# Kernel optimization log

Measured on AMD Instinct MI355X. Metric: run time of the kernel, lower is better.

## Reference

```python
import jax, jax.numpy as jnp
import numpy as np

B, N, C = 2, 2048, 256
H_DIM, W_DIM = 64, 176


def _lin_init(k, fan_in, shape):
    return jax.random.normal(k, shape, dtype=jnp.float32) * (1.0 / np.sqrt(fan_in))


def setup_inputs() -> dict:
    key = jax.random.key(0)
    ks = jax.random.split(key, 12)
    # gaussian_data: (B, N, 14); positions [:3], sigma_x at 5, sigma_y at 6, weight at 12
    z = jax.random.uniform(ks[0], (B, N), minval=1.0, maxval=40.0)
    x = jax.random.uniform(ks[1], (B, N), minval=-0.6, maxval=0.6) * z
    y = jax.random.uniform(ks[2], (B, N), minval=-0.4, maxval=0.4) * z
    g = jax.random.normal(ks[3], (B, N, 14), dtype=jnp.float32)
    g = g.at[..., 0].set(x).at[..., 1].set(y).at[..., 2].set(z)
    g = g.at[..., 5].set(jax.random.uniform(ks[4], (B, N), minval=5.0, maxval=50.0))
    g = g.at[..., 6].set(jax.random.uniform(ks[5], (B, N), minval=5.0, maxval=50.0))
    g = g.at[..., 12].set(jax.random.uniform(ks[6], (B, N), minval=0.5, maxval=1.5))
    # pinhole intrinsic: fx=fy=1000, cx=880, cy=320
    intrinsic = jnp.array([[1000.0, 0.0, 880.0], [0.0, 1000.0, 320.0], [0.0, 0.0, 1.0]], dtype=jnp.float32)
    pk = jax.random.split(ks[7], 5)
    return {
        "gaussian_data": g,
        "intrinsic": intrinsic,
        "enc_w1": _lin_init(pk[0], 14, (14, 64)), "enc_b1": jnp.zeros((64,), jnp.float32),
        "enc_w2": _lin_init(pk[1], 64, (64, 128)), "enc_b2": jnp.zeros((128,), jnp.float32),
        "enc_w3": _lin_init(pk[2], 128, (128, C)), "enc_b3": jnp.zeros((C,), jnp.float32),
        "ft_w1": _lin_init(pk[3], C, (C, C)), "ft_b1": jnp.zeros((C,), jnp.float32),
        "ft_w2": _lin_init(pk[4], C, (C, C)), "ft_b2": jnp.zeros((C,), jnp.float32),
        "H": H_DIM, "W": W_DIM,
    }


def reference(gaussian_data, intrinsic, enc_w1, enc_b1, enc_w2, enc_b2, enc_w3, enc_b3,
              ft_w1, ft_b1, ft_w2, ft_b2, H, W):
    # Encoder MLP (dropout = identity in eval): (B,N,14) -> (B,N,C)
    h = jax.nn.relu(gaussian_data @ enc_w1 + enc_b1)
    h = jax.nn.relu(h @ enc_w2 + enc_b2)
    feats = h @ enc_w3 + enc_b3
    # feature_transform inside GaussianRadarProjection
    feats_t = jax.nn.relu(feats @ ft_w1 + ft_b1) @ ft_w2 + ft_b2  # (B,N,C)

    pos = gaussian_data[..., :3]                      # (B,N,3)
    valid = pos[..., 2] > 0.1                         # (B,N)
    proj = jnp.einsum('ij,bnj->bni', intrinsic, pos)  # (B,N,3)
    pts2d = proj[..., :2] / (proj[..., 2:3] + 1e-6)   # (B,N,2)
    scale_x = W / intrinsic[0, 2] / 2
    scale_y = H / intrinsic[1, 2] / 2
    px = pts2d[..., 0] * scale_x                      # (B,N)
    py = pts2d[..., 1] * scale_y
    inb = (px >= 0) & (px < W) & (py >= 0) & (py < H)
    mask = valid & inb                                # (B,N)

    sx = jnp.maximum(gaussian_data[..., 5] * scale_x, 1.0)  # (B,N)
    sy = jnp.maximum(gaussian_data[..., 6] * scale_y, 1.0)
    w = gaussian_data[..., 12]                               # (B,N)

    xg = jnp.arange(W, dtype=jnp.float32)
    yg = jnp.arange(H, dtype=jnp.float32)
    dx2 = ((xg[None, None, :] - px[..., None]) / sx[..., None]) ** 2  # (B,N,W)
    dy2 = ((yg[None, None, :] - py[..., None]) / sy[..., None]) ** 2  # (B,N,H)
    dist = dy2[..., :, None] + dx2[..., None, :]                      # (B,N,H,W)
    gw = jnp.exp(-0.5 * dist) * w[..., None, None]
    gw = gw * (dist < 9.0).astype(gw.dtype) * mask[..., None, None].astype(gw.dtype)

    density = jnp.sum(gw, axis=1)[:, None]                             # (B,1,H,W)
    feature_map = jnp.einsum('bnc,bnhw->bchw', feats_t, gw)            # (B,C,H,W)
    avg_sigma = (sx + sy) / 2                                          # (B,N)
    uncertainty = jnp.sum(gw * avg_sigma[..., None, None], axis=1)[:, None]

    density = jnp.clip(density, 1e-6)
    return feature_map / density, uncertainty / density, density
```

## Files before the change

### kernel.cpp

```cpp
#include <hip/hip_runtime.h>
#include <cstdint>
#include <cstddef>

#define B_ 2
#define N_ 2048
#define C_ 256
#define H_ 64
#define W_ 176
#define TW 16
#define NTX 11
#define NYB 32
#define NTILES2 (B_*NYB*NTX)
#define NSUB 8
#define SUBCAP 256
#define SA 260
#define FS 40
#define CSTRIDE 16

typedef unsigned short ushort_t;
typedef short bf16x8 __attribute__((ext_vector_type(8)));
typedef float f32x4  __attribute__((ext_vector_type(4)));

__device__ __forceinline__ short f2bf(float f)
{
    unsigned u = __float_as_uint(f);
    return (short)((u + 0x7FFFu + ((u >> 16) & 1u)) >> 16);
}

__global__ __launch_bounds__(256)
void prep_kernel(const float* __restrict__ w3f, const float* __restrict__ fw1f,
                 const float* __restrict__ fw2f,
                 short* __restrict__ wt3, short* __restrict__ wt4,
                 short* __restrict__ wt5, int* __restrict__ counts)
{
    const int gid = blockIdx.x * 256 + threadIdx.x;
    for (int c = gid; c < NTILES2 * NSUB * CSTRIDE; c += 65536) counts[c] = 0;
    for (int e = gid; e < 163840; e += 65536) {
        if (e < 32768) {
            const int k = e >> 8, n = e & 255;
            wt3[n * 128 + k] = f2bf(w3f[e]);
        } else if (e < 98304) {
            const int e2 = e - 32768;
            const int k = e2 >> 8, n = e2 & 255;
            wt4[n * 256 + k] = f2bf(fw1f[e2]);
        } else {
            const int e2 = e - 98304;
            const int k = e2 >> 8, n = e2 & 255;
            wt5[n * 256 + k] = f2bf(fw2f[e2]);
        }
    }
}

template<int K>
__device__ __forceinline__ void mfma_acc(const short* __restrict__ wt,
                                         const float* actIn, f32x4 (&acc)[2],
                                         int wv_, int quad, int ln15)
{
    bf16x8 wreg[K / 16];
#pragma unroll
    for (int ks = 0; ks < K / 32; ++ks) {
        const int kb = ks * 32 + quad * 8;
#pragma unroll
        for (int tt = 0; tt < 2; ++tt) {
            const int n0 = (wv_ * 2 + tt) * 16;
            wreg[ks * 2 + tt] = *(const bf16x8*)&wt[(size_t)(n0 + ln15) * K + kb];
        }
    }
#pragma unroll
    for (int ks = 0; ks < K / 32; ++ks) {
        const int kb = ks * 32 + quad * 8;
        const float4 a0 = *(const float4*)&actIn[ln15 * SA + kb];
        const float4 a1 = *(const float4*)&actIn[ln15 * SA + kb + 4];
        bf16x8 af = { f2bf(a0.x), f2bf(a0.y), f2bf(a0.z), f2bf(a0.w),
                      f2bf(a1.x), f2bf(a1.y), f2bf(a1.z), f2bf(a1.w) };
#pragma unroll
        for (int tt = 0; tt < 2; ++tt)
            acc[tt] = __builtin_amdgcn_mfma_f32_16x16x32_bf16(af, wreg[ks * 2 + tt],
                                                              acc[tt], 0, 0, 0);
    }
}

__global__ __launch_bounds__(512, 4)
void pb_mlp_kernel(const float* __restrict__ g, const float* __restrict__ intr,
                   const float* __restrict__ w1, const float* __restrict__ b1,
                   const float* __restrict__ w2, const float* __restrict__ b2,
                   const short* __restrict__ wt3, const float* __restrict__ b3,
                   const short* __restrict__ wt4, const float* __restrict__ fb1,
                   const short* __restrict__ wt5, const float* __restrict__ fb2,
                   ushort_t* __restrict__ ftb,
                   float* __restrict__ pp, int* __restrict__ counts,
                   ushort_t* __restrict__ lists)
{
    __shared__ __align__(16) float A_[16 * SA];
    __shared__ __align__(16) float Bb[16 * SA];
    const int tid = threadIdx.x;

    if (blockIdx.x < 256) {
        const int row0 = blockIdx.x * 16;
        const int lane = tid & 63;
        const int wv_  = tid >> 6;
        const int quad = lane >> 4;
        const int ln15 = lane & 15;

        if (tid < 224) {
            const int k = tid / 16, m = tid % 16;
            A_[m * SA + k] = g[(size_t)(row0 + m) * 14 + k];
        }
        __syncthreads();

        {
            const int col = tid & 63;
            const int m0  = (tid >> 6) * 2;
            float acc[2];
            const float bv = b1[col];
            acc[0] = bv; acc[1] = bv;
#pragma unroll
            for (int k = 0; k < 14; ++k) {
                const float wv = w1[k * 64 + col];
                acc[0] = fmaf(A_[(m0 + 0) * SA + k], wv, acc[0]);
                acc[1] = fmaf(A_[(m0 + 1) * SA + k], wv, acc[1]);
            }
            Bb[(m0 + 0) * SA + col] = fmaxf(acc[0], 0.f);
            Bb[(m0 + 1) * SA + col] = fmaxf(acc[1], 0.f);
        }
        __syncthreads();

        {
            const int col = tid & 127;
            const int m0  = (tid >> 7) * 4;
            float acc[4];
            const float bv = b2[col];
#pragma unroll
            for (int r = 0; r < 4; ++r) acc[r] = bv;
#pragma unroll 4
            for (int kq = 0; kq < 16; ++kq) {
                float wv[4];
#pragma unroll
                for (int jj = 0; jj < 4; ++jj) wv[jj] = w2[(4 * kq + jj) * 128 + col];
#pragma unroll
                for (int r = 0; r < 4; ++r) {
                    const float4 a4 = *(const float4*)&Bb[(m0 + r) * SA + 4 * kq];
                    acc[r] = fmaf(a4.x, wv[0], acc[r]);
                    acc[r] = fmaf(a4.y, wv[1], acc[r]);
                    acc[r] = fmaf(a4.z, wv[2], acc[r]);
                    acc[r] = fmaf(a4.w, wv[3], acc[r]);
                }
            }
#pragma unroll
            for (int r = 0; r < 4; ++r)
                A_[(m0 + r) * SA + col] = fmaxf(acc[r], 0.f);
        }
        __syncthreads();

        {
            f32x4 acc[2] = {{0,0,0,0},{0,0,0,0}};
            mfma_acc<128>(wt3, A_, acc, wv_, quad, ln15);
            __syncthreads();
#pragma unroll
            for (int tt = 0; tt < 2; ++tt) {
                const int n = (wv_ * 2 + tt) * 16 + ln15;
                const float bv = b3[n];
#pragma unroll
                for (int r = 0; r < 4; ++r)
                    Bb[(quad * 4 + r) * SA + n] = acc[tt][r] + bv;
            }
        }
        __syncthreads();

        {
            f32x4 acc[2] = {{0,0,0,0},{0,0,0,0}};
            mfma_acc<256>(wt4, Bb, acc, wv_, quad, ln15);
            __syncthreads();
#pragma unroll
            for (int tt = 0; tt < 2; ++tt) {
                const int n = (wv_ * 2 + tt) * 16 + ln15;
                const float bv = fb1[n];
#pragma unroll
                for (int r = 0; r < 4; ++r)
                    A_[(quad * 4 + r) * SA + n] = fmaxf(acc[tt][r] + bv, 0.f);
            }
        }
        __syncthreads();

        {
            f32x4 acc[2] = {{0,0,0,0},{0,0,0,0}};
            mfma_acc<256>(wt5, A_, acc, wv_, quad, ln15);
#pragma unroll
            for (int tt = 0; tt < 2; ++tt) {
                const int n = (wv_ * 2 + tt) * 16 + ln15;
                const float bv = fb2[n];
#pragma unroll
                for (int r = 0; r < 4; ++r)
                    ftb[(size_t)(row0 + quad * 4 + r) * 256 + n] =
                        (ushort_t)f2bf(acc[tt][r] + bv);
            }
        }
        return;
    }

    const int sub = (blockIdx.x - 256) & (NSUB - 1);
    const int i = (blockIdx.x - 256) * 16 + (tid >> 5);
    const int j = tid & 31;
    const float* gi = g + (size_t)i * 14;
    const float x = gi[0], y = gi[1], z = gi[2];
    const float s5 = gi[5], s6 = gi[6], wv = gi[12];
    const float k00 = intr[0], k01 = intr[1], k02 = intr[2];
    const float k10 = intr[3], k11 = intr[4], k12 = intr[5];
    const float k20 = intr[6], k21 = intr[7], k22 = intr[8];
    const float projx = k00 * x + k01 * y + k02 * z;
    const float projy = k10 * x + k11 * y + k12 * z;
    const float projz = k20 * x + k21 * y + k22 * z;
    const float inv = 1.f / (projz + 1e-6f);
    const float scale_x = (float)W_ / k02 * 0.5f;
    const float scale_y = (float)H_ / k12 * 0.5f;
    const float px = projx * inv * scale_x;
    const float py = projy * inv * scale_y;
    const bool valid = z > 0.1f;
    const bool inb = (px >= 0.f) && (px < (float)W_) && (py >= 0.f) && (py < (float)H_);
    const bool mask = valid && inb;
    const float sx = fmaxf(s5 * scale_x, 1.f);
    const float sy = fmaxf(s6 * scale_y, 1.f);
    if (j == 0) {
        float4* o = (float4*)(pp + (size_t)i * 8);
        o[0] = make_float4(px, py, 1.f / sx, 1.f / sy);
        o[1] = make_float4(wv, 0.5f * (sx + sy), 0.f, 0.f);
    }
    if (!mask) return;
    const float rx = 3.f * sx, ry = 3.f * sy;
    const int ymin = max(0, (int)floorf(py - ry));
    const int ymax = min(H_ - 1, (int)ceilf(py + ry));
    const int bmin = ymin >> 1, bmax = ymax >> 1;
    const int band = bmin + j;
    if (band > bmax) return;
    const int tmin = max(0, (int)floorf((px - rx - (float)(TW - 1)) * (1.f / TW)));
    const int tmax = min(NTX - 1, (int)ceilf((px + rx) * (1.f / TW)));
    const int b = i / N_, n = i - b * N_;
    for (int t = tmin; t <= tmax; ++t) {
        const int tile = (b * NYB + band) * NTX + t;
        const int slot = atomicAdd(&counts[(tile * NSUB + sub) * CSTRIDE], 1);
        if (slot < SUBCAP)
            lists[((size_t)tile * NSUB + sub) * SUBCAP + slot] = (ushort_t)n;
    }
}

__global__ __launch_bounds__(512)
void splat_kernel(const float* __restrict__ pp, const ushort_t* __restrict__ lists,
                  const int* __restrict__ counts, const ushort_t* __restrict__ ftb,
                  float* __restrict__ out)
{
    __shared__ __align__(16) ushort_t feats_t[2][256 * FS];
    __shared__ __align__(16) ushort_t gw_t[2][32 * FS];
    __shared__ __align__(16) ushort_t list_s[NSUB * SUBCAP];

    const int tid = threadIdx.x;
    const int qb = blockIdx.x;
    const int b  = qb & 1;
    const int t_ = qb >> 1;
    const int yr = t_ / NTX, xr = t_ % NTX;
    const int yh = (yr + 1) >> 1;
    const int yb = (yr & 1) ? (16 - yh) : (16 + yh);
    const int xh = (xr + 1) >> 1;
    const int txi = (xr & 1) ? (5 - xh) : (5 + xh);
    const int tb  = (b * NYB + yb) * NTX + txi;
    const int y0 = yb * 2, x0 = txi * TW;

    int cs[NSUB];
#pragma unroll
    for (int s = 0; s < NSUB; ++s)
        cs[s] = min(counts[(tb * NSUB + s) * CSTRIDE], SUBCAP);
    int off[NSUB];
    int tot = 0;
#pragma unroll
    for (int s = 0; s < NSUB; ++s) { off[s] = tot; tot += cs[s]; }
#pragma unroll
    for (int s = 0; s < NSUB; ++s) {
        const ushort_t* src = lists + ((size_t)tb * NSUB + s) * SUBCAP;
        if (tid < cs[s]) list_s[off[s] + tid] = src[tid];
    }
    __syncthreads();
    const int cnt = tot;

    const ushort_t* mylist = list_s;
    const int gs   = tid >> 5;
    const int px32 = tid & 31;
    const float fy = (float)(y0 + (px32 >> 4));
    const float fx = (float)(x0 + (px32 & 15));
    const int chg = tid >> 4;
    const int qp  = tid & 15;
    const int bN = b * N_;
    const int lane = tid & 63;
    const int wv_  = tid >> 6;
    const int quad = lane >> 4;
    const int ln15 = lane & 15;

    f32x4 acc[2][2];
#pragma unroll
    for (int mt = 0; mt < 2; ++mt)
#pragma unroll
        for (int nt = 0; nt < 2; ++nt) acc[mt][nt] = (f32x4){0.f, 0.f, 0.f, 0.f};
    float densp = 0.f, uncp = 0.f;

    uint4 ra0, rb0;
    const int nchunks = (cnt + 31) >> 5;

    if (cnt > 0) {
        const float4* pv = (const float4*)pp;
        {
            const int n0 = mylist[min(2 * qp, cnt - 1)];
            const int n1 = mylist[min(2 * qp + 1, cnt - 1)];
            ra0 = *(const uint4*)(ftb + ((size_t)(bN + n0) << 8) + chg * 8);
            rb0 = *(const uint4*)(ftb + ((size_t)(bN + n1) << 8) + chg * 8);
        }
        for (int c = 0; c < nchunks; ++c) {
            const int buf = c & 1;
#pragma unroll
            for (int jj = 0; jj < 2; ++jj) {
                const int q = 16 * jj + gs;
                const int qi = c * 32 + q;
                const int n = mylist[min(qi, cnt - 1)];
                const float4 e0 = pv[(size_t)(bN + n) * 2 + 0];
                const float4 e1 = pv[(size_t)(bN + n) * 2 + 1];
                const float dyn = (fy - e0.y) * e0.w;
                const float dxn = (fx - e0.x) * e0.z;
                const float dist = dyn * dyn + dxn * dxn;
                float gv = 0.f;
                if (dist < 9.f) gv = __expf(-0.5f * dist) * e1.x;
                if (qi >= cnt) gv = 0.f;
                gw_t[buf][px32 * FS + q] = (ushort_t)f2bf(gv);
                densp += gv;
                uncp  += gv * e1.y;
            }
            {
                uint* dst = (uint*)&feats_t[buf][0];
#pragma unroll
                for (int jj = 0; jj < 4; ++jj) {
                    const uint u0 = (&ra0.x)[jj], v0 = (&rb0.x)[jj];
                    const int ch = chg * 8 + 2 * jj;
                    dst[ch * (FS / 2) + qp]       = (u0 & 0xffffu) | (v0 << 16);
                    dst[(ch + 1) * (FS / 2) + qp] = (u0 >> 16) | (v0 & 0xffff0000u);
                }
            }
            __syncthreads();
            if (c + 1 < nchunks) {
                const int q0 = (c + 1) * 32 + 2 * qp;
                const int n0 = mylist[min(q0, cnt - 1)];
                const int n1 = mylist[min(q0 + 1, cnt - 1)];
                ra0 = *(const uint4*)(ftb + ((size_t)(bN + n0) << 8) + chg * 8);
                rb0 = *(const uint4*)(ftb + ((size_t)(bN + n1) << 8) + chg * 8);
            }
            bf16x8 af[2];
#pragma unroll
            for (int mt = 0; mt < 2; ++mt)
                af[mt] = *(const bf16x8*)&gw_t[buf][(mt * 16 + ln15) * FS + quad * 8];
#pragma unroll
            for (int nt = 0; nt < 2; ++nt) {
                const int ch0 = wv_ * 32 + nt * 16;
                const bf16x8 bf = *(const bf16x8*)&feats_t[buf][(ch0 + ln15) * FS + quad * 8];
                acc[0][nt] = __builtin_amdgcn_mfma_f32_16x16x32_bf16(af[0], bf, acc[0][nt], 0, 0, 0);
                acc[1][nt] = __builtin_amdgcn_mfma_f32_16x16x32_bf16(af[1], bf, acc[1][nt], 0, 0, 0);
            }
        }
    }

    __syncthreads();
    float* red_d = (float*)&feats_t[0][0];
    float* red_u = red_d + 16 * 36;
    red_d[gs * 36 + px32] = densp;
    red_u[gs * 36 + px32] = uncp;
    __syncthreads();
    for (int s = 8; s > 0; s >>= 1) {
        if (gs < s) {
            red_d[gs * 36 + px32] += red_d[(gs + s) * 36 + px32];
            red_u[gs * 36 + px32] += red_u[(gs + s) * 36 + px32];
        }
        __syncthreads();
    }

    if (tid < 32) {
        const int yy = y0 + (tid >> 4), xx = x0 + (tid & 15);
        const size_t pix = ((size_t)b * H_ + yy) * W_ + xx;
        float* unc_o = out + (size_t)B_ * C_ * H_ * W_;
        float* den_o = unc_o + (size_t)B_ * H_ * W_;
        const float d = fmaxf(red_d[tid], 1e-6f);
        unc_o[pix] = red_u[tid] / d;
        den_o[pix] = d;
    }

#pragma unroll
    for (int mt = 0; mt < 2; ++mt) {
        const int pxb = mt * 16 + quad * 4;
        float rinv[4];
#pragma unroll
        for (int r = 0; r < 4; ++r)
            rinv[r] = 1.f / fmaxf(red_d[pxb + r], 1e-6f);
        const int yy = y0 + mt;
#pragma unroll
        for (int nt = 0; nt < 2; ++nt) {
            const int ch = wv_ * 32 + nt * 16 + ln15;
            float4 v;
            v.x = acc[mt][nt][0] * rinv[0];
            v.y = acc[mt][nt][1] * rinv[1];
            v.z = acc[mt][nt][2] * rinv[2];
            v.w = acc[mt][nt][3] * rinv[3];
            *(float4*)(out + (((size_t)b * C_ + ch) * H_ + yy) * W_
                       + x0 + quad * 4) = v;
        }
    }
}

extern "C" void kernel_launch(void* const* d_in, const int* in_sizes, int n_in,
                              void* d_out, int out_size, void* d_ws, size_t ws_size,
                              hipStream_t stream)
{
    const float* g    = (const float*)d_in[0];
    const float* intr = (const float*)d_in[1];
    const float* w1   = (const float*)d_in[2];
    const float* b1   = (const float*)d_in[3];
    const float* w2   = (const float*)d_in[4];
    const float* b2   = (const float*)d_in[5];
    const float* w3   = (const float*)d_in[6];
    const float* b3   = (const float*)d_in[7];
    const float* fw1  = (const float*)d_in[8];
    const float* fb1  = (const float*)d_in[9];
    const float* fw2  = (const float*)d_in[10];
    const float* fb2  = (const float*)d_in[11];

    char* base = (char*)d_ws;
    const int rows = B_ * N_;
    ushort_t* ftb = (ushort_t*)base;
    float* pp     = (float*)(base + (size_t)rows * C_ * 2);
    int*   counts = (int*)(pp + (size_t)8 * rows);
    ushort_t* lists = (ushort_t*)(counts + NTILES2 * NSUB * CSTRIDE);
    short* wt3    = (short*)(lists + (size_t)NTILES2 * NSUB * SUBCAP);
    short* wt4    = wt3 + 128 * 256;
    short* wt5    = wt4 + 256 * 256;

    prep_kernel<<<dim3(256), dim3(256), 0, stream>>>(w3, fw1, fw2, wt3, wt4, wt5, counts);
    pb_mlp_kernel<<<dim3(512), dim3(512), 0, stream>>>(
        g, intr, w1, b1, w2, b2, wt3, b3, wt4, fb1, wt5, fb2, ftb, pp, counts, lists);
    splat_kernel<<<dim3(NTILES2), dim3(512), 0, stream>>>(pp, lists, counts, ftb, (float*)d_out);
}
```

Measured before the change: 128.8 us.

## Store MLP activations as bf16 in LDS and deepen splat prefetch pipeline

The MLP kernel now keeps its intermediate activations in shared memory as bf16 with a padded stride. This removes the per-load float-to-bf16 conversions and halves the LDS footprint, which also lets two __syncthreads calls be dropped. The splat kernel gains a 4-wave occupancy hint and prefetches feature rows two chunks ahead with register double-buffering. It also prefetches the next chunk's gaussian parameters into registers while the current chunk is being processed. The extra in-flight registers may cost occupancy, and the drop from two barriers to one between MLP stages depends on the separate buffer alternation being safe.

```diff
diff --git a/kernel.cpp b/kernel.cpp
--- a/kernel.cpp
+++ b/kernel.cpp
@@ -13,9 +13,9 @@
 #define NTILES2 (B_*NYB*NTX)
 #define NSUB 8
 #define SUBCAP 256
-#define SA 260
 #define FS 40
 #define CSTRIDE 16
+#define SAB 264
 
 typedef unsigned short ushort_t;
 typedef short bf16x8 __attribute__((ext_vector_type(8)));
@@ -52,9 +52,9 @@
 }
 
 template<int K>
-__device__ __forceinline__ void mfma_acc(const short* __restrict__ wt,
-                                         const float* actIn, f32x4 (&acc)[2],
-                                         int wv_, int quad, int ln15)
+__device__ __forceinline__ void mfma_accB(const short* __restrict__ wt,
+                                          const ushort_t* actB, f32x4 (&acc)[2],
+                                          int wv_, int quad, int ln15)
 {
     bf16x8 wreg[K / 16];
 #pragma unroll
@@ -69,10 +69,7 @@
 #pragma unroll
     for (int ks = 0; ks < K / 32; ++ks) {
         const int kb = ks * 32 + quad * 8;
-        const float4 a0 = *(const float4*)&actIn[ln15 * SA + kb];
-        const float4 a1 = *(const float4*)&actIn[ln15 * SA + kb + 4];
-        bf16x8 af = { f2bf(a0.x), f2bf(a0.y), f2bf(a0.z), f2bf(a0.w),
-                      f2bf(a1.x), f2bf(a1.y), f2bf(a1.z), f2bf(a1.w) };
+        const bf16x8 af = *(const bf16x8*)&actB[ln15 * SAB + kb];
 #pragma unroll
         for (int tt = 0; tt < 2; ++tt)
             acc[tt] = __builtin_amdgcn_mfma_f32_16x16x32_bf16(af, wreg[ks * 2 + tt],
@@ -91,8 +88,10 @@
                    float* __restrict__ pp, int* __restrict__ counts,
                    ushort_t* __restrict__ lists)
 {
-    __shared__ __align__(16) float A_[16 * SA];
-    __shared__ __align__(16) float Bb[16 * SA];
+    __shared__ __align__(16) float   s32a[16 * 16];
+    __shared__ __align__(16) float   s32b[16 * 68];
+    __shared__ __align__(16) ushort_t bA[16 * SAB];
+    __shared__ __align__(16) ushort_t bB[16 * SAB];
     const int tid = threadIdx.x;
 
     if (blockIdx.x < 256) {
@@ -104,7 +103,7 @@
 
         if (tid < 224) {
             const int k = tid / 16, m = tid % 16;
-            A_[m * SA + k] = g[(size_t)(row0 + m) * 14 + k];
+            s32a[m * 16 + k] = g[(size_t)(row0 + m) * 14 + k];
         }
         __syncthreads();
 
@@ -117,11 +116,11 @@
 #pragma unroll
             for (int k = 0; k < 14; ++k) {
                 const float wv = w1[k * 64 + col];
-                acc[0] = fmaf(A_[(m0 + 0) * SA + k], wv, acc[0]);
-                acc[1] = fmaf(A_[(m0 + 1) * SA + k], wv, acc[1]);
-            }
-            Bb[(m0 + 0) * SA + col] = fmaxf(acc[0], 0.f);
-            Bb[(m0 + 1) * SA + col] = fmaxf(acc[1], 0.f);
+                acc[0] = fmaf(s32a[(m0 + 0) * 16 + k], wv, acc[0]);
+                acc[1] = fmaf(s32a[(m0 + 1) * 16 + k], wv, acc[1]);
+            }
+            s32b[(m0 + 0) * 68 + col] = fmaxf(acc[0], 0.f);
+            s32b[(m0 + 1) * 68 + col] = fmaxf(acc[1], 0.f);
         }
         __syncthreads();
 
@@ -139,7 +138,7 @@
                 for (int jj = 0; jj < 4; ++jj) wv[jj] = w2[(4 * kq + jj) * 128 + col];
 #pragma unroll
                 for (int r = 0; r < 4; ++r) {
-                    const float4 a4 = *(const float4*)&Bb[(m0 + r) * SA + 4 * kq];
+                    const float4 a4 = *(const float4*)&s32b[(m0 + r) * 68 + 4 * kq];
                     acc[r] = fmaf(a4.x, wv[0], acc[r]);
                     acc[r] = fmaf(a4.y, wv[1], acc[r]);
                     acc[r] = fmaf(a4.z, wv[2], acc[r]);
@@ -148,43 +147,42 @@
             }
 #pragma unroll
             for (int r = 0; r < 4; ++r)
-                A_[(m0 + r) * SA + col] = fmaxf(acc[r], 0.f);
+                bA[(m0 + r) * SAB + col] = (ushort_t)f2bf(fmaxf(acc[r], 0.f));
         }
         __syncthreads();
 
         {
             f32x4 acc[2] = {{0,0,0,0},{0,0,0,0}};
-            mfma_acc<128>(wt3, A_, acc, wv_, quad, ln15);
-            __syncthreads();
+            mfma_accB<128>(wt3, bA, acc, wv_, quad, ln15);
 #pragma unroll
             for (int tt = 0; tt < 2; ++tt) {
                 const int n = (wv_ * 2 + tt) * 16 + ln15;
                 const float bv = b3[n];
 #pragma unroll
                 for (int r = 0; r < 4; ++r)
-                    Bb[(quad * 4 + r) * SA + n] = acc[tt][r] + bv;
+                    bB[(quad * 4 + r) * SAB + n] = (ushort_t)f2bf(acc[tt][r] + bv);
             }
         }
         __syncthreads();
 
         {
             f32x4 acc[2] = {{0,0,0,0},{0,0,0,0}};
-            mfma_acc<256>(wt4, Bb, acc, wv_, quad, ln15);
-            __syncthreads();
+            mfma_accB<256>(wt4, bB, acc, wv_, quad, ln15);
 #pragma unroll
             for (int tt = 0; tt < 2; ++tt) {
                 const int n = (wv_ * 2 + tt) * 16 + ln15;
                 const float bv = fb1[n];
 #pragma unroll
                 for (int r = 0; r < 4; ++r)
-                    A_[(quad * 4 + r) * SA + n] = fmaxf(acc[tt][r] + bv, 0.f);
+                    bA[(quad * 4 + r) * SAB + n] =
+                        (ushort_t)f2bf(fmaxf(acc[tt][r] + bv, 0.f));
             }
         }
         __syncthreads();
 
         {
             f32x4 acc[2] = {{0,0,0,0},{0,0,0,0}};
-            mfma_acc<256>(wt5, A_, acc, wv_, quad, ln15);
+            mfma_accB<256>(wt5, bA, acc, wv_, quad, ln15);
 #pragma unroll
             for (int tt = 0; tt < 2; ++tt) {
                 const int n = (wv_ * 2 + tt) * 16 + ln15;
@@ -243,7 +241,7 @@
     }
 }
 
-__global__ __launch_bounds__(512)
+__global__ __launch_bounds__(512, 4)
 void splat_kernel(const float* __restrict__ pp, const ushort_t* __restrict__ lists,
                   const int* __restrict__ counts, const ushort_t* __restrict__ ftb,
                   float* __restrict__ out)
@@ -280,7 +278,6 @@
     __syncthreads();
     const int cnt = tot;
 
-    const ushort_t* mylist = list_s;
     const int gs   = tid >> 5;
     const int px32 = tid & 31;
     const float fy = (float)(y0 + (px32 >> 4));
@@ -300,26 +297,40 @@
         for (int nt = 0; nt < 2; ++nt) acc[mt][nt] = (f32x4){0.f, 0.f, 0.f, 0.f};
     float densp = 0.f, uncp = 0.f;
 
-    uint4 ra0, rb0;
+    uint4 fa[2], fb[2];
+    float4 pe0[2], pe1[2];
     const int nchunks = (cnt + 31) >> 5;
 
     if (cnt > 0) {
         const float4* pv = (const float4*)pp;
         {
-            const int n0 = mylist[min(2 * qp, cnt - 1)];
-            const int n1 = mylist[min(2 * qp + 1, cnt - 1)];
-            ra0 = *(const uint4*)(ftb + ((size_t)(bN + n0) << 8) + chg * 8);
-            rb0 = *(const uint4*)(ftb + ((size_t)(bN + n1) << 8) + chg * 8);
-        }
+            const int n0 = list_s[min(2 * qp, cnt - 1)];
+            const int n1 = list_s[min(2 * qp + 1, cnt - 1)];
+            fa[0] = *(const uint4*)(ftb + ((size_t)(bN + n0) << 8) + chg * 8);
+            fb[0] = *(const uint4*)(ftb + ((size_t)(bN + n1) << 8) + chg * 8);
+        }
+        if (nchunks > 1) {
+            const int q0 = 32 + 2 * qp;
+            const int n0 = list_s[min(q0, cnt - 1)];
+            const int n1 = list_s[min(q0 + 1, cnt - 1)];
+            fa[1] = *(const uint4*)(ftb + ((size_t)(bN + n0) << 8) + chg * 8);
+            fb[1] = *(const uint4*)(ftb + ((size_t)(bN + n1) << 8) + chg * 8);
+        }
+#pragma unroll
+        for (int jj = 0; jj < 2; ++jj) {
+            const int n = list_s[min(16 * jj + gs, cnt - 1)];
+            pe0[jj] = pv[(size_t)(bN + n) * 2 + 0];
+            pe1[jj] = pv[(size_t)(bN + n) * 2 + 1];
+        }
+
         for (int c = 0; c < nchunks; ++c) {
             const int buf = c & 1;
 #pragma unroll
             for (int jj = 0; jj < 2; ++jj) {
                 const int q = 16 * jj + gs;
                 const int qi = c * 32 + q;
-                const int n = mylist[min(qi, cnt - 1)];
-                const float4 e0 = pv[(size_t)(bN + n) * 2 + 0];
-                const float4 e1 = pv[(size_t)(bN + n) * 2 + 1];
+                const float4 e0 = pe0[jj];
+                const float4 e1 = pe1[jj];
                 const float dyn = (fy - e0.y) * e0.w;
                 const float dxn = (fx - e0.x) * e0.z;
                 const float dist = dyn * dyn + dxn * dxn;
@@ -330,23 +341,33 @@
                 densp += gv;
                 uncp  += gv * e1.y;
             }
+            if (c + 1 < nchunks) {
+#pragma unroll
+                for (int jj = 0; jj < 2; ++jj) {
+                    const int qi = (c + 1) * 32 + 16 * jj + gs;
+                    const int n = list_s[min(qi, cnt - 1)];
+                    pe0[jj] = pv[(size_t)(bN + n) * 2 + 0];
+                    pe1[jj] = pv[(size_t)(bN + n) * 2 + 1];
+                }
+            }
             {
                 uint* dst = (uint*)&feats_t[buf][0];
+                const uint4 ua = fa[buf], ub = fb[buf];
 #pragma unroll
                 for (int jj = 0; jj < 4; ++jj) {
-                    const uint u0 = (&ra0.x)[jj], v0 = (&rb0.x)[jj];
+                    const uint u0 = (&ua.x)[jj], v0 = (&ub.x)[jj];
                     const int ch = chg * 8 + 2 * jj;
                     dst[ch * (FS / 2) + qp]       = (u0 & 0xffffu) | (v0 << 16);
                     dst[(ch + 1) * (FS / 2) + qp] = (u0 >> 16) | (v0 & 0xffff0000u);
                 }
             }
             __syncthreads();
-            if (c + 1 < nchunks) {
-                const int q0 = (c + 1) * 32 + 2 * qp;
-                const int n0 = mylist[min(q0, cnt - 1)];
-                const int n1 = mylist[min(q0 + 1, cnt - 1)];
-                ra0 = *(const uint4*)(ftb + ((size_t)(bN + n0) << 8) + chg * 8);
-                rb0 = *(const uint4*)(ftb + ((size_t)(bN + n1) << 8) + chg * 8);
+            if (c + 2 < nchunks) {
+                const int q0 = (c + 2) * 32 + 2 * qp;
+                const int n0 = list_s[min(q0, cnt - 1)];
+                const int n1 = list_s[min(q0 + 1, cnt - 1)];
+                fa[buf] = *(const uint4*)(ftb + ((size_t)(bN + n0) << 8) + chg * 8);
+                fb[buf] = *(const uint4*)(ftb + ((size_t)(bN + n1) << 8) + chg * 8);
             }
             bf16x8 af[2];
 #pragma unroll
@@ -355,9 +376,9 @@
 #pragma unroll
             for (int nt = 0; nt < 2; ++nt) {
                 const int ch0 = wv_ * 32 + nt * 16;
-                const bf16x8 bf = *(const bf16x8*)&feats_t[buf][(ch0 + ln15) * FS + quad * 8];
-                acc[0][nt] = __builtin_amdgcn_mfma_f32_16x16x32_bf16(af[0], bf, acc[0][nt], 0, 0, 0);
-                acc[1][nt] = __builtin_amdgcn_mfma_f32_16x16x32_bf16(af[1], bf, acc[1][nt], 0, 0, 0);
+                const bf16x8 bfv = *(const bf16x8*)&feats_t[buf][(ch0 + ln15) * FS + quad * 8];
+                acc[0][nt] = __builtin_amdgcn_mfma_f32_16x16x32_bf16(af[0], bfv, acc[0][nt], 0, 0, 0);
+                acc[1][nt] = __builtin_amdgcn_mfma_f32_16x16x32_bf16(af[1], bfv, acc[1][nt], 0, 0, 0);
             }
         }
     }
```

After: 148.4 us. 15.3% more time.
